# Kernel optimization log

Hardware: AMD Instinct MI355X
Metric: run time of the kernel (lower is better)

## Reference

```python
import jax, jax.numpy as jnp
import numpy as np

WK = 5        # fine_window_size
STRIDE = 4    # hardcoded in forward
PAD = WK // 2


def _gather_windows(feat, b, idx):
    # feat: [N, C, H, W]; b, idx: [M]. Replicates F.unfold(k=5, s=4, p=2)
    # followed by permute/reshape(n, l, W^2, c) and advanced indexing,
    # but only materializes the M selected windows (fused unfold+gather).
    N, C, H, W = feat.shape
    out_w = (W + 2 * PAD - WK) // STRIDE + 1
    fp = jnp.pad(feat, ((0, 0), (0, 0), (PAD, PAD), (PAD, PAD)))
    gy = idx // out_w
    gx = idx % out_w
    rows = gy[:, None] * STRIDE + jnp.arange(WK)   # [M, WK]
    cols = gx[:, None] * STRIDE + jnp.arange(WK)   # [M, WK]
    # advanced indices at axes 0,2,3 with slice at axis 1 -> [M, WK, WK, C]
    patch = fp[b[:, None, None], :, rows[:, :, None], cols[:, None, :]]
    # F.unfold flattens channel-major (C, kh, kw); the torch code then
    # reshapes that C*WK*WK axis as (WK*WK, C) -- an index-mixing reshape
    # we must replicate exactly.
    M = b.shape[0]
    patch = patch.transpose(0, 3, 1, 2).reshape(M, C * WK * WK)
    return patch.reshape(M, WK * WK, C)


def setup_inputs() -> dict:
    key = jax.random.key(0)
    k0, k1, kb, ki, kj = jax.random.split(key, 5)
    N, C, H, W = 4, 128, 240, 320
    L = (H // STRIDE) * (W // STRIDE)  # 4800 coarse positions
    M = 6000
    return {
        "feat_f0": jax.random.normal(k0, (N, C, H, W), dtype=jnp.float32),
        "feat_f1": jax.random.normal(k1, (N, C, H, W), dtype=jnp.float32),
        "hw0_f": jnp.array([H, W], dtype=jnp.int64),
        "hw0_c": jnp.array([H // STRIDE, W // STRIDE], dtype=jnp.int64),
        "b_ids": jax.random.randint(kb, (M,), 0, N, dtype=jnp.int64),
        "i_ids": jax.random.randint(ki, (M,), 0, L, dtype=jnp.int64),
        "j_ids": jax.random.randint(kj, (M,), 0, L, dtype=jnp.int64),
    }


def reference(feat_f0, feat_f1, hw0_f, hw0_c, b_ids, i_ids, j_ids):
    feat0 = _gather_windows(feat_f0, b_ids, i_ids)  # [M, W^2, C]
    feat1 = _gather_windows(feat_f1, b_ids, j_ids)  # [M, W^2, C]
    return feat0, feat1
```

## Files before the change

### kernel.cpp

```cpp
#include <hip/hip_runtime.h>


#define MPTS 6000
#define NCH  128
#define FH   240
#define FW   320
#define OUTW 80
#define PTFLOATS (NCH * 25)

typedef float f2 __attribute__((ext_vector_type(2)));

__global__ __launch_bounds__(320) void fine_gather_kernel(
    const float* __restrict__ f0, const float* __restrict__ f1,
    const int* __restrict__ b_ids, const int* __restrict__ i_ids,
    const int* __restrict__ j_ids, float* __restrict__ out)
{
    __shared__ __align__(16) float lds[PTFLOATS];

    const int blk = blockIdx.x;
    const int map = blk >= MPTS;
    const int m   = map ? blk - MPTS : blk;
    const float* __restrict__ feat = map ? f1 : f0;
    const int idx = map ? j_ids[m] : i_ids[m];
    const int b   = b_ids[m];

    const int gy = idx / OUTW;
    const int gx = idx - gy * OUTW;
    const int row0 = gy * 4 - 2;
    const int col0 = gx * 4 - 2;

    const int t = threadIdx.x;

#pragma unroll
    for (int it = 0; it < 2; it++) {
        const int s = t + it * 320;
        const int c = s / 5;
        const int r = s - c * 5;
        const int row = row0 + r;
        const bool vrow = (row >= 0) & (row < FH);
        const float* src = feat + (((long)(b * NCH + c) * FH + row) * FW + col0);

        float v[5];
        if (vrow && (col0 >= 0)) {
            const f2* p = (const f2*)src;
            f2 a0 = p[0];
            f2 a1 = p[1];
            v[0] = a0.x; v[1] = a0.y; v[2] = a1.x; v[3] = a1.y;
            v[4] = src[4];
        } else {
#pragma unroll
            for (int k = 0; k < 5; k++) {
                const int cc = col0 + k;
                v[k] = (vrow && cc >= 0) ? src[k] : 0.0f;
            }
        }
        const int base = s * 5;
#pragma unroll
        for (int k = 0; k < 5; k++) lds[base + k] = v[k];
    }

    __syncthreads();

    float4* __restrict__ dst = (float4*)(out + (long)blk * PTFLOATS);
    const float4* sl = (const float4*)lds;
    for (int i = t; i < PTFLOATS / 4; i += 320)
        dst[i] = sl[i];
}

extern "C" void kernel_launch(void* const* d_in, const int* in_sizes, int n_in,
                              void* d_out, int out_size, void* d_ws, size_t ws_size,
                              hipStream_t stream) {
    const float* f0   = (const float*)d_in[0];
    const float* f1   = (const float*)d_in[1];
    const int* b_ids  = (const int*)d_in[4];
    const int* i_ids  = (const int*)d_in[5];
    const int* j_ids  = (const int*)d_in[6];
    float* out        = (float*)d_out;

    fine_gather_kernel<<<2 * MPTS, 320, 0, stream>>>(f0, f1, b_ids, i_ids, j_ids, out);
}
```

Baseline: 438.2 us.

## Counting-sort gather jobs by spatial key for cache locality, nontemporal output stores

Adds a counting-sort prepass (zero histogram, atomic histogram, single-block scan, scatter) that orders the gather jobs by (map, batch, grid index). Blocks with nearby windows then run close together, so overlapping 5x5 windows and shared cache lines are reused in L2/MALL. Output stores become nontemporal so the large write stream does not evict the feature data. This costs four extra small launches, including a serial single-block scan over 38400 bins, and the sorted order is not deterministic because it comes from atomics.

```diff
diff --git a/kernel.cpp b/kernel.cpp
--- a/kernel.cpp
+++ b/kernel.cpp
@@ -1,25 +1,90 @@
 #include <hip/hip_runtime.h>
 
 
-#define MPTS 6000
-#define NCH  128
-#define FH   240
-#define FW   320
-#define OUTW 80
+#define MPTS  6000
+#define NCH   128
+#define FH    240
+#define FW    320
+#define OUTW  80
+#define LGRID 4800
+#define NJOBS (2 * MPTS)
+#define NBINS (2 * 4 * LGRID)
 #define PTFLOATS (NCH * 25)
 
 typedef float f2 __attribute__((ext_vector_type(2)));
+typedef float f4 __attribute__((ext_vector_type(4)));
+
+
+__global__ __launch_bounds__(256) void zero_hist_k(int* __restrict__ h) {
+    int i = blockIdx.x * 256 + threadIdx.x;
+    if (i < NBINS) h[i] = 0;
+}
+
+__device__ __forceinline__ int job_key(int j, const int* b_ids,
+                                       const int* i_ids, const int* j_ids) {
+    int map = j >= MPTS;
+    int m   = map ? j - MPTS : j;
+    int idx = map ? j_ids[m] : i_ids[m];
+    return map * (4 * LGRID) + b_ids[m] * LGRID + idx;
+}
+
+__global__ __launch_bounds__(256) void hist_k(
+    const int* __restrict__ b_ids, const int* __restrict__ i_ids,
+    const int* __restrict__ j_ids, int* __restrict__ h) {
+    int j = blockIdx.x * 256 + threadIdx.x;
+    if (j >= NJOBS) return;
+    atomicAdd(&h[job_key(j, b_ids, i_ids, j_ids)], 1);
+}
+
+__global__ __launch_bounds__(1024) void scan_k(int* __restrict__ h) {
+    __shared__ int sums[1024];
+    const int t = threadIdx.x;
+    const int per = (NBINS + 1023) / 1024;
+    const int base = t * per;
+    int vals[38];
+    int local = 0;
+#pragma unroll
+    for (int k = 0; k < per; k++) {
+        int i = base + k;
+        int v = (i < NBINS) ? h[i] : 0;
+        vals[k] = v; local += v;
+    }
+    sums[t] = local;
+    __syncthreads();
+    for (int off = 1; off < 1024; off <<= 1) {
+        int v = (t >= off) ? sums[t - off] : 0;
+        __syncthreads();
+        sums[t] += v;
+        __syncthreads();
+    }
+    int excl = (t == 0) ? 0 : sums[t - 1];
+#pragma unroll
+    for (int k = 0; k < per; k++) {
+        int i = base + k;
+        if (i < NBINS) { h[i] = excl; excl += vals[k]; }
+    }
+}
+
+__global__ __launch_bounds__(256) void scatter_k(
+    const int* __restrict__ b_ids, const int* __restrict__ i_ids,
+    const int* __restrict__ j_ids, int* __restrict__ h, int* __restrict__ sorted) {
+    int j = blockIdx.x * 256 + threadIdx.x;
+    if (j >= NJOBS) return;
+    int pos = atomicAdd(&h[job_key(j, b_ids, i_ids, j_ids)], 1);
+    sorted[pos] = j;
+}
 
 __global__ __launch_bounds__(320) void fine_gather_kernel(
     const float* __restrict__ f0, const float* __restrict__ f1,
     const int* __restrict__ b_ids, const int* __restrict__ i_ids,
-    const int* __restrict__ j_ids, float* __restrict__ out)
+    const int* __restrict__ j_ids, const int* __restrict__ sorted,
+    float* __restrict__ out)
 {
     __shared__ __align__(16) float lds[PTFLOATS];
 
-    const int blk = blockIdx.x;
-    const int map = blk >= MPTS;
-    const int m   = map ? blk - MPTS : blk;
+    const int job = sorted[blockIdx.x];
+    const int map = job >= MPTS;
+    const int m   = map ? job - MPTS : job;
     const float* __restrict__ feat = map ? f1 : f0;
     const int idx = map ? j_ids[m] : i_ids[m];
     const int b   = b_ids[m];
@@ -61,10 +126,10 @@
 
     __syncthreads();
 
-    float4* __restrict__ dst = (float4*)(out + (long)blk * PTFLOATS);
-    const float4* sl = (const float4*)lds;
+    f4* __restrict__ dst = (f4*)(out + (long)job * PTFLOATS);
+    const f4* sl = (const f4*)lds;
     for (int i = t; i < PTFLOATS / 4; i += 320)
-        dst[i] = sl[i];
+        __builtin_nontemporal_store(sl[i], &dst[i]);
 }
 
 extern "C" void kernel_launch(void* const* d_in, const int* in_sizes, int n_in,
@@ -77,5 +142,12 @@
     const int* j_ids  = (const int*)d_in[6];
     float* out        = (float*)d_out;
 
-    fine_gather_kernel<<<2 * MPTS, 320, 0, stream>>>(f0, f1, b_ids, i_ids, j_ids, out);
+    int* hist   = (int*)d_ws;
+    int* sorted = hist + NBINS;
+
+    zero_hist_k<<<(NBINS + 255) / 256, 256, 0, stream>>>(hist);
+    hist_k<<<(NJOBS + 255) / 256, 256, 0, stream>>>(b_ids, i_ids, j_ids, hist);
+    scan_k<<<1, 1024, 0, stream>>>(hist);
+    scatter_k<<<(NJOBS + 255) / 256, 256, 0, stream>>>(b_ids, i_ids, j_ids, hist, sorted);
+    fine_gather_kernel<<<NJOBS, 320, 0, stream>>>(f0, f1, b_ids, i_ids, j_ids, sorted, out);
 }
```

New measurement: 448.5 us. 1.02x slower.
